# Kernel optimization log

Measured on AMD Instinct MI355X. Metric: run time of the kernel, lower is better.

## Reference

```python
import jax, jax.numpy as jnp
import numpy as np

INPUT_DIM = 1024
CODEBOOK_DIM = 128
CODEBOOK_SIZE = 8192
B, N = 8, 4096


def setup_inputs() -> dict:
    key = jax.random.key(0)
    k1, k2, k3 = jax.random.split(key, 3)
    x = jax.random.normal(k1, (B, N, INPUT_DIM), dtype=jnp.float32)
    # xavier_normal_: std = sqrt(2 / (fan_in + fan_out))
    xavier_std = float(np.sqrt(2.0 / (INPUT_DIM + CODEBOOK_DIM)))
    random_projection = jax.random.normal(k2, (INPUT_DIM, CODEBOOK_DIM), dtype=jnp.float32) * xavier_std
    codebook = jax.random.normal(k3, (CODEBOOK_SIZE, CODEBOOK_DIM), dtype=jnp.float32)
    return {"x": x, "random_projection": random_projection, "codebook": codebook}


def reference(x, random_projection, codebook):
    # random projection: [B, N, D] @ [D, E] -> [B, N, E]
    proj = jnp.einsum("bnd,de->bne", x, random_projection)
    b, n, e = proj.shape
    flat = proj.reshape(b * n, e)  # [BN, E]
    eps = 1e-12  # matches torch F.normalize default eps
    nx = flat / jnp.maximum(jnp.linalg.norm(flat, axis=1, keepdims=True), eps)
    ncb = codebook / jnp.maximum(jnp.linalg.norm(codebook, axis=1, keepdims=True), eps)
    # squared euclidean distances [K, BN]; argmin of d^2 == argmin of cdist
    d2 = (
        jnp.sum(ncb * ncb, axis=1)[:, None]
        + jnp.sum(nx * nx, axis=1)[None, :]
        - 2.0 * (ncb @ nx.T)
    )
    nearest = jnp.argmin(d2, axis=0)  # [BN]
    return nearest.reshape(b, n).astype(jnp.int32)
```

## Files before the change

### kernel.cpp

```cpp
#include <hip/hip_runtime.h>
#include <math.h>
#include <float.h>
#include <limits.h>

#define BN      32768
#define D_IN    1024
#define E_DIM   128
#define CB_N    8192

typedef _Float16 f16x8 __attribute__((ext_vector_type(8)));
typedef _Float16 f16x4 __attribute__((ext_vector_type(4)));
typedef float    f32x4 __attribute__((ext_vector_type(4)));


__global__ __launch_bounds__(256) void pack_cb_kernel(
    const float* __restrict__ cb, _Float16* __restrict__ ph,
    _Float16* __restrict__ pl) {
    __shared__ float L[16][129];
    const int t = threadIdx.x;
    const int g = blockIdx.x;

    const int c = t >> 4, p = t & 15;
    const float4 v0 = *(const float4*)&cb[(size_t)(g * 16 + c) * E_DIM + p * 8];
    const float4 v1 = *(const float4*)&cb[(size_t)(g * 16 + c) * E_DIM + p * 8 + 4];
    float ss = v0.x * v0.x + v0.y * v0.y + v0.z * v0.z + v0.w * v0.w
             + v1.x * v1.x + v1.y * v1.y + v1.z * v1.z + v1.w * v1.w;
#pragma unroll
    for (int m = 1; m < 16; m <<= 1) ss += __shfl_xor(ss, m);
    const float inv = 256.0f / fmaxf(sqrtf(ss), 1e-12f);

    L[c][p * 8 + 0] = v0.x * inv; L[c][p * 8 + 1] = v0.y * inv;
    L[c][p * 8 + 2] = v0.z * inv; L[c][p * 8 + 3] = v0.w * inv;
    L[c][p * 8 + 4] = v1.x * inv; L[c][p * 8 + 5] = v1.y * inv;
    L[c][p * 8 + 6] = v1.z * inv; L[c][p * 8 + 7] = v1.w * inv;
    __syncthreads();

    const int kb = t >> 6, lane = t & 63;
    const int quad = (lane >> 4), col = lane & 15;
    f16x8 h, l;
#pragma unroll
    for (int j = 0; j < 8; ++j) {
        const float v = L[col][kb * 32 + quad * 8 + j];
        const _Float16 hv = (_Float16)v;
        h[j] = hv;
        l[j] = (_Float16)(v - (float)hv);
    }
    const size_t off = ((size_t)(g * 4 + kb) * 64 + lane) * 8;
    *(f16x8*)&ph[off] = h;
    *(f16x8*)&pl[off] = l;
}

__global__ __launch_bounds__(256) void proj_kernel(
    const float* __restrict__ x, const float* __restrict__ rp,
    _Float16* __restrict__ qh, _Float16* __restrict__ ql) {
    __shared__ float As[32][68];
    __shared__ float Bs[32][128];

    const int tid = threadIdx.x;
    const int tx  = tid & 15;
    const int ty  = tid >> 4;
    const int rbase = blockIdx.x * 64;

    float acc[4][8];
#pragma unroll
    for (int i = 0; i < 4; ++i)
#pragma unroll
        for (int j = 0; j < 8; ++j) acc[i][j] = 0.0f;

    for (int kb = 0; kb < D_IN; kb += 32) {
#pragma unroll
        for (int i = 0; i < 2; ++i) {
            const int flat = tid + i * 256;
            const int r  = flat >> 3;
            const int kc = (flat & 7) * 4;
            const float4 a = *(const float4*)&x[(size_t)(rbase + r) * D_IN + kb + kc];
            As[kc + 0][r] = a.x;
            As[kc + 1][r] = a.y;
            As[kc + 2][r] = a.z;
            As[kc + 3][r] = a.w;
        }
#pragma unroll
        for (int i = 0; i < 4; ++i) {
            const int flat = tid + i * 256;
            const int kk = flat >> 5;
            const int e4 = (flat & 31) * 4;
            *(float4*)&Bs[kk][e4] = *(const float4*)&rp[(size_t)(kb + kk) * E_DIM + e4];
        }
        __syncthreads();

#pragma unroll
        for (int k = 0; k < 32; ++k) {
            const float4 av = *(const float4*)&As[k][ty * 4];
            const float4 b0 = *(const float4*)&Bs[k][tx * 4];
            const float4 b1 = *(const float4*)&Bs[k][tx * 4 + 64];
            const float a_[4] = {av.x, av.y, av.z, av.w};
            const float b_[8] = {b0.x, b0.y, b0.z, b0.w, b1.x, b1.y, b1.z, b1.w};
#pragma unroll
            for (int qi = 0; qi < 4; ++qi)
#pragma unroll
                for (int ci = 0; ci < 8; ++ci)
                    acc[qi][ci] = fmaf(a_[qi], b_[ci], acc[qi][ci]);
        }
        __syncthreads();
    }

#pragma unroll
    for (int ri = 0; ri < 4; ++ri) {
        const int row = rbase + ty * 4 + ri;
        _Float16 h[8], l[8];
#pragma unroll
        for (int j = 0; j < 8; ++j) {
            const float v = acc[ri][j] * 16.0f;
            const _Float16 hv = (_Float16)v;
            h[j] = hv;
            l[j] = (_Float16)(v - (float)hv);
        }
        f16x4 h0 = {h[0], h[1], h[2], h[3]}, h1 = {h[4], h[5], h[6], h[7]};
        f16x4 l0 = {l[0], l[1], l[2], l[3]}, l1 = {l[4], l[5], l[6], l[7]};
        *(f16x4*)&qh[(size_t)row * E_DIM + tx * 4]      = h0;
        *(f16x4*)&qh[(size_t)row * E_DIM + 64 + tx * 4] = h1;
        *(f16x4*)&ql[(size_t)row * E_DIM + tx * 4]      = l0;
        *(f16x4*)&ql[(size_t)row * E_DIM + 64 + tx * 4] = l1;
    }
}

__global__ __launch_bounds__(256, 2) void scores_kernel(
    const _Float16* __restrict__ qh, const _Float16* __restrict__ ql,
    const _Float16* __restrict__ ph, const _Float16* __restrict__ pl,
    int* __restrict__ out) {
    __shared__ float ls[4][64];
    __shared__ int   li[4][64];

    const int tid  = threadIdx.x;
    const int w    = tid >> 6;
    const int lane = tid & 63;
    const int quad = lane >> 4, col = lane & 15;
    const int qb   = blockIdx.x * 64;

    f16x8 ah[4][4], al[4][4];
#pragma unroll
    for (int mt = 0; mt < 4; ++mt)
#pragma unroll
        for (int kb = 0; kb < 4; ++kb) {
            const size_t off = (size_t)(qb + mt * 16 + col) * E_DIM + kb * 32 + quad * 8;
            ah[mt][kb] = *(const f16x8*)&qh[off];
            al[mt][kb] = *(const f16x8*)&ql[off];
        }

    float bs[16];
    int   bi[16];
#pragma unroll
    for (int s = 0; s < 16; ++s) { bs[s] = -FLT_MAX; bi[s] = 0; }

    const int g0 = w * (CB_N / 16 / 4);
    for (int t = 0; t < CB_N / 16 / 4; ++t) {
        const int g = g0 + t;
        f16x8 bh[4], bl[4];
#pragma unroll
        for (int kb = 0; kb < 4; ++kb) {
            const size_t off = ((size_t)(g * 4 + kb) * 64 + lane) * 8;
            bh[kb] = *(const f16x8*)&ph[off];
            bl[kb] = *(const f16x8*)&pl[off];
        }

        f32x4 acc[4];
#pragma unroll
        for (int mt = 0; mt < 4; ++mt) acc[mt] = (f32x4){0.f, 0.f, 0.f, 0.f};

#pragma unroll
        for (int kb = 0; kb < 4; ++kb)
#pragma unroll
            for (int mt = 0; mt < 4; ++mt)
                acc[mt] = __builtin_amdgcn_mfma_f32_16x16x32_f16(ah[mt][kb], bh[kb], acc[mt], 0, 0, 0);
#pragma unroll
        for (int kb = 0; kb < 4; ++kb)
#pragma unroll
            for (int mt = 0; mt < 4; ++mt)
                acc[mt] = __builtin_amdgcn_mfma_f32_16x16x32_f16(ah[mt][kb], bl[kb], acc[mt], 0, 0, 0);
#pragma unroll
        for (int kb = 0; kb < 4; ++kb)
#pragma unroll
            for (int mt = 0; mt < 4; ++mt)
                acc[mt] = __builtin_amdgcn_mfma_f32_16x16x32_f16(al[mt][kb], bh[kb], acc[mt], 0, 0, 0);

        const int code = g * 16 + col;
#pragma unroll
        for (int mt = 0; mt < 4; ++mt)
#pragma unroll
            for (int r = 0; r < 4; ++r) {
                const float v = acc[mt][r];
                const int s = mt * 4 + r;
                if (v > bs[s]) { bs[s] = v; bi[s] = code; }
            }
    }

#pragma unroll
    for (int s = 0; s < 16; ++s) {
#pragma unroll
        for (int m = 1; m < 16; m <<= 1) {
            const float os = __shfl_xor(bs[s], m);
            const int   oi = __shfl_xor(bi[s], m);
            if (os > bs[s] || (os == bs[s] && oi < bi[s])) { bs[s] = os; bi[s] = oi; }
        }
    }

    if (col == 0) {
#pragma unroll
        for (int mt = 0; mt < 4; ++mt)
#pragma unroll
            for (int r = 0; r < 4; ++r) {
                ls[w][mt * 16 + quad * 4 + r] = bs[mt * 4 + r];
                li[w][mt * 16 + quad * 4 + r] = bi[mt * 4 + r];
            }
    }
    __syncthreads();

    if (tid < 64) {
        float s = ls[0][tid];
        int   i = li[0][tid];
#pragma unroll
        for (int ww = 1; ww < 4; ++ww) {
            const float os = ls[ww][tid];
            const int   oi = li[ww][tid];
            if (os > s) { s = os; i = oi; }
        }
        out[qb + tid] = i;
    }
}

extern "C" void kernel_launch(void* const* d_in, const int* in_sizes, int n_in,
                              void* d_out, int out_size, void* d_ws, size_t ws_size,
                              hipStream_t stream) {
    const float* x  = (const float*)d_in[0];
    const float* rp = (const float*)d_in[1];
    const float* cb = (const float*)d_in[2];
    int* out = (int*)d_out;

    _Float16* qh = (_Float16*)d_ws;
    _Float16* ql = qh + (size_t)BN * E_DIM;
    _Float16* ph = ql + (size_t)BN * E_DIM;
    _Float16* pl = ph + (size_t)CB_N * E_DIM;

    pack_cb_kernel<<<CB_N / 16, 256, 0, stream>>>(cb, ph, pl);
    proj_kernel<<<BN / 64, 256, 0, stream>>>(x, rp, qh, ql);
    scores_kernel<<<BN / 64, 256, 0, stream>>>(qh, ql, ph, pl, out);
}
```

Baseline: 465.0 us.

## Move projection GEMM to split-fp16 MFMA with prepacked projection matrix

Replaces the FP32 FMA projection GEMM with MFMA f16 instructions, using a hi/lo fp16 split (three MFMAs per tile) to keep near-fp32 accuracy. A new small kernel prepacks the random projection into MFMA fragment layout with scaling. The x tile is converted to hi/lo fp16 in padded LDS, and the next global load is software-prefetched into registers. This targets the compute cost of the 32768x1024x128 projection, at the price of an extra launch, scaling tricks that could affect argmin ties, and scalar stores of the output.

```diff
diff --git a/kernel.cpp b/kernel.cpp
--- a/kernel.cpp
+++ b/kernel.cpp
@@ -50,77 +50,130 @@
     *(f16x8*)&pl[off] = l;
 }
 
+__global__ __launch_bounds__(64) void pack_rp_kernel(
+    const float* __restrict__ rp, _Float16* __restrict__ rph,
+    _Float16* __restrict__ rpl) {
+    const int b = blockIdx.x;
+    const int kb = b >> 3, nt = b & 7;
+    const int lane = threadIdx.x;
+    const int quad = lane >> 4, col = lane & 15;
+    f16x8 h, l;
+#pragma unroll
+    for (int j = 0; j < 8; ++j) {
+        const float v = rp[(size_t)(kb * 32 + quad * 8 + j) * E_DIM + nt * 16 + col] * 64.0f;
+        const _Float16 hv = (_Float16)v;
+        h[j] = hv;
+        l[j] = (_Float16)(v - (float)hv);
+    }
+    const size_t off = ((size_t)b * 64 + lane) * 8;
+    *(f16x8*)&rph[off] = h;
+    *(f16x8*)&rpl[off] = l;
+}
+
+#define PAD_ROW 40
+
 __global__ __launch_bounds__(256) void proj_kernel(
-    const float* __restrict__ x, const float* __restrict__ rp,
+    const float* __restrict__ x,
+    const _Float16* __restrict__ rph, const _Float16* __restrict__ rpl,
     _Float16* __restrict__ qh, _Float16* __restrict__ ql) {
-    __shared__ float As[32][68];
-    __shared__ float Bs[32][128];
-
-    const int tid = threadIdx.x;
-    const int tx  = tid & 15;
-    const int ty  = tid >> 4;
+    __shared__ _Float16 Ah[64 * PAD_ROW];
+    __shared__ _Float16 Al[64 * PAD_ROW];
+
+    const int tid  = threadIdx.x;
+    const int lane = tid & 63;
+    const int w    = tid >> 6;
+    const int quad = lane >> 4, col = lane & 15;
     const int rbase = blockIdx.x * 64;
 
-    float acc[4][8];
-#pragma unroll
-    for (int i = 0; i < 4; ++i)
-#pragma unroll
-        for (int j = 0; j < 8; ++j) acc[i][j] = 0.0f;
-
-    for (int kb = 0; kb < D_IN; kb += 32) {
+    const int srow = tid >> 3;
+    const int skc  = (tid & 7) * 4;
+
+    f32x4 acc[4][2];
+#pragma unroll
+    for (int mt = 0; mt < 4; ++mt)
+#pragma unroll
+        for (int h = 0; h < 2; ++h) acc[mt][h] = (f32x4){0.f, 0.f, 0.f, 0.f};
+
+    float4 pre[2];
+#pragma unroll
+    for (int i = 0; i < 2; ++i)
+        pre[i] = *(const float4*)&x[(size_t)(rbase + srow + 32 * i) * D_IN + skc];
+
+    for (int kb = 0; kb < 32; ++kb) {
 #pragma unroll
         for (int i = 0; i < 2; ++i) {
-            const int flat = tid + i * 256;
-            const int r  = flat >> 3;
-            const int kc = (flat & 7) * 4;
-            const float4 a = *(const float4*)&x[(size_t)(rbase + r) * D_IN + kb + kc];
-            As[kc + 0][r] = a.x;
-            As[kc + 1][r] = a.y;
-            As[kc + 2][r] = a.z;
-            As[kc + 3][r] = a.w;
-        }
-#pragma unroll
-        for (int i = 0; i < 4; ++i) {
-            const int flat = tid + i * 256;
-            const int kk = flat >> 5;
-            const int e4 = (flat & 31) * 4;
-            *(float4*)&Bs[kk][e4] = *(const float4*)&rp[(size_t)(kb + kk) * E_DIM + e4];
+            const float vv[4] = {pre[i].x, pre[i].y, pre[i].z, pre[i].w};
+            f16x4 h4, l4;
+#pragma unroll
+            for (int j = 0; j < 4; ++j) {
+                const float v = vv[j] * 512.0f;
+                const _Float16 hv = (_Float16)v;
+                h4[j] = hv;
+                l4[j] = (_Float16)(v - (float)hv);
+            }
+            const int base = (srow + 32 * i) * PAD_ROW + skc;
+            *(f16x4*)&Ah[base] = h4;
+            *(f16x4*)&Al[base] = l4;
         }
         __syncthreads();
 
-#pragma unroll
-        for (int k = 0; k < 32; ++k) {
-            const float4 av = *(const float4*)&As[k][ty * 4];
-            const float4 b0 = *(const float4*)&Bs[k][tx * 4];
-            const float4 b1 = *(const float4*)&Bs[k][tx * 4 + 64];
-            const float a_[4] = {av.x, av.y, av.z, av.w};
-            const float b_[8] = {b0.x, b0.y, b0.z, b0.w, b1.x, b1.y, b1.z, b1.w};
-#pragma unroll
-            for (int qi = 0; qi < 4; ++qi)
-#pragma unroll
-                for (int ci = 0; ci < 8; ++ci)
-                    acc[qi][ci] = fmaf(a_[qi], b_[ci], acc[qi][ci]);
-        }
+        if (kb + 1 < 32) {
+#pragma unroll
+            for (int i = 0; i < 2; ++i)
+                pre[i] = *(const float4*)&x[(size_t)(rbase + srow + 32 * i) * D_IN + (kb + 1) * 32 + skc];
+        }
+
+        f16x8 bh[2], bl[2];
+#pragma unroll
+        for (int h = 0; h < 2; ++h) {
+            const int nt = w * 2 + h;
+            const size_t off = ((size_t)(kb * 8 + nt) * 64 + lane) * 8;
+            bh[h] = *(const f16x8*)&rph[off];
+            bl[h] = *(const f16x8*)&rpl[off];
+        }
+
+        f16x8 ah[4], al[4];
+#pragma unroll
+        for (int mt = 0; mt < 4; ++mt) {
+            const int base = (mt * 16 + col) * PAD_ROW + quad * 8;
+            ah[mt] = *(const f16x8*)&Ah[base];
+            al[mt] = *(const f16x8*)&Al[base];
+        }
+
+#pragma unroll
+        for (int mt = 0; mt < 4; ++mt)
+#pragma unroll
+            for (int h = 0; h < 2; ++h)
+                acc[mt][h] = __builtin_amdgcn_mfma_f32_16x16x32_f16(ah[mt], bh[h], acc[mt][h], 0, 0, 0);
+#pragma unroll
+        for (int mt = 0; mt < 4; ++mt)
+#pragma unroll
+            for (int h = 0; h < 2; ++h)
+                acc[mt][h] = __builtin_amdgcn_mfma_f32_16x16x32_f16(ah[mt], bl[h], acc[mt][h], 0, 0, 0);
+#pragma unroll
+        for (int mt = 0; mt < 4; ++mt)
+#pragma unroll
+            for (int h = 0; h < 2; ++h)
+                acc[mt][h] = __builtin_amdgcn_mfma_f32_16x16x32_f16(al[mt], bh[h], acc[mt][h], 0, 0, 0);
+
         __syncthreads();
     }
 
 #pragma unroll
-    for (int ri = 0; ri < 4; ++ri) {
-        const int row = rbase + ty * 4 + ri;
-        _Float16 h[8], l[8];
-#pragma unroll
-        for (int j = 0; j < 8; ++j) {
-            const float v = acc[ri][j] * 16.0f;
-            const _Float16 hv = (_Float16)v;
-            h[j] = hv;
-            l[j] = (_Float16)(v - (float)hv);
-        }
-        f16x4 h0 = {h[0], h[1], h[2], h[3]}, h1 = {h[4], h[5], h[6], h[7]};
-        f16x4 l0 = {l[0], l[1], l[2], l[3]}, l1 = {l[4], l[5], l[6], l[7]};
-        *(f16x4*)&qh[(size_t)row * E_DIM + tx * 4]      = h0;
-        *(f16x4*)&qh[(size_t)row * E_DIM + 64 + tx * 4] = h1;
-        *(f16x4*)&ql[(size_t)row * E_DIM + tx * 4]      = l0;
-        *(f16x4*)&ql[(size_t)row * E_DIM + 64 + tx * 4] = l1;
+    for (int mt = 0; mt < 4; ++mt) {
+#pragma unroll
+        for (int h = 0; h < 2; ++h) {
+#pragma unroll
+            for (int r = 0; r < 4; ++r) {
+                const float v = acc[mt][h][r] * (1.0f / 2048.0f);
+                const _Float16 hv = (_Float16)v;
+                const _Float16 lv = (_Float16)(v - (float)hv);
+                const size_t o = (size_t)(rbase + mt * 16 + quad * 4 + r) * E_DIM
+                               + w * 32 + h * 16 + col;
+                qh[o] = hv;
+                ql[o] = lv;
+            }
+        }
     }
 }
 
@@ -221,8 +274,7 @@
 #pragma unroll
         for (int ww = 1; ww < 4; ++ww) {
             const float os = ls[ww][tid];
-            const int   oi = li[ww][tid];
-            if (os > s) { s = os; i = oi; }
+            if (os > s) { s = os; i = li[ww][tid]; }
         }
         out[qb + tid] = i;
     }
@@ -236,12 +288,15 @@
     const float* cb = (const float*)d_in[2];
     int* out = (int*)d_out;
 
-    _Float16* qh = (_Float16*)d_ws;
-    _Float16* ql = qh + (size_t)BN * E_DIM;
-    _Float16* ph = ql + (size_t)BN * E_DIM;
-    _Float16* pl = ph + (size_t)CB_N * E_DIM;
+    _Float16* qh  = (_Float16*)d_ws;
+    _Float16* ql  = qh  + (size_t)BN * E_DIM;
+    _Float16* ph  = ql  + (size_t)BN * E_DIM;
+    _Float16* pl  = ph  + (size_t)CB_N * E_DIM;
+    _Float16* rph = pl  + (size_t)CB_N * E_DIM;
+    _Float16* rpl = rph + (size_t)D_IN * E_DIM;
 
     pack_cb_kernel<<<CB_N / 16, 256, 0, stream>>>(cb, ph, pl);
-    proj_kernel<<<BN / 64, 256, 0, stream>>>(x, rp, qh, ql);
+    pack_rp_kernel<<<256, 64, 0, stream>>>(rp, rph, rpl);
+    proj_kernel<<<BN / 64, 256, 0, stream>>>(x, rph, rpl, qh, ql);
     scores_kernel<<<BN / 64, 256, 0, stream>>>(qh, ql, ph, pl, out);
 }
```

New measurement: 419.4 us. 9.8% less time.
